# Performance work log

Hardware: AMD Instinct MI355X
Metric: run time of the kernel (lower is better)

Reference implementation:

```python
import jax, jax.numpy as jnp
import numpy as np

B, N, D, H = 2, 2048, 1024, 16
DH = D // H
MASK_VALUE = -1e7


def setup_inputs() -> dict:
    key = jax.random.key(0)
    ks = jax.random.split(key, 8)
    scale = 0.02
    return {
        "queries": jax.random.normal(ks[0], (B, N, D), dtype=jnp.float32),
        "keys": jax.random.normal(ks[1], (B, N, D), dtype=jnp.float32),
        "values": jax.random.normal(ks[2], (B, N, D), dtype=jnp.float32),
        "valid_len": jax.random.randint(ks[3], (B * H,), 1, N + 1, dtype=jnp.int32),
        "Wq": jax.random.normal(ks[4], (D, D), dtype=jnp.float32) * scale,
        "Wk": jax.random.normal(ks[5], (D, D), dtype=jnp.float32) * scale,
        "Wv": jax.random.normal(ks[6], (D, D), dtype=jnp.float32) * scale,
        "Wo": jax.random.normal(ks[7], (D, D), dtype=jnp.float32) * scale,
    }


def reference(queries, keys, values, valid_len, Wq, Wk, Wv, Wo):
    b, n, d = queries.shape
    h, dh = H, d // H

    def split_heads(x):  # (b, n, d) -> (b, h, n, dh)
        return x.reshape(b, n, h, dh).transpose(0, 2, 1, 3)

    q = split_heads(queries @ Wq)
    k = split_heads(keys @ Wk)
    v = split_heads(values @ Wv)

    # (b, h, nq, nk) full score tensor, as in the original naive bmm path
    scores = jnp.einsum("bhqd,bhkd->bhqk", q, k) / jnp.sqrt(jnp.float32(dh))

    # valid_len is 1-D of length b*h; repeat_interleave over queries means the
    # mask depends only on the key index: keep k < valid_len[bh]
    vl = valid_len.reshape(b, h, 1, 1)
    keep = jnp.arange(n)[None, None, None, :] < vl  # (b, h, 1, nk)
    scores = jnp.where(keep, scores, MASK_VALUE)

    attn = jax.nn.softmax(scores, axis=-1)
    heads = jnp.einsum("bhqk,bhkd->bhqd", attn, v)  # (b, h, n, dh)
    out = heads.transpose(0, 2, 1, 3).reshape(b, n, d) @ Wo
    return out
```

## Files before the change

kernel.cpp:

```cpp
#include <hip/hip_runtime.h>

#define B_ 2
#define N_ 2048
#define D_ 1024
#define H_ 16
#define DH_ 64
#define NITEMS 1024

typedef _Float16 half8 __attribute__((ext_vector_type(8)));
typedef _Float16 half4 __attribute__((ext_vector_type(4)));
typedef float f32x4 __attribute__((ext_vector_type(4)));

__device__ __forceinline__ void gl2lds16(const _Float16* g, _Float16* l) {
  __builtin_amdgcn_global_load_lds(
      (const __attribute__((address_space(1))) void*)g,
      (__attribute__((address_space(3))) void*)l, 16, 0, 0);
}

__global__ __launch_bounds__(256) void prep_kernel(
    const float* __restrict__ q, const float* __restrict__ k,
    const float* __restrict__ v, const float* __restrict__ Wq,
    const float* __restrict__ Wk, const float* __restrict__ Wv,
    const float* __restrict__ Wo, const int* __restrict__ vlen,
    _Float16* __restrict__ Xf, _Float16* __restrict__ WtAll,
    int* __restrict__ order) {
  __shared__ float tile[64][65];
  const int bid = blockIdx.x;
  if (bid < 6144) {
    int y = bid >> 11, x = bid & 2047;
    const float* s = (y == 0) ? q : (y == 1) ? k : v;
    _Float16* d = Xf + (size_t)y * ((size_t)B_ * N_ * D_);
    size_t idx = ((size_t)x * 256 + threadIdx.x) * 8;
    float4 a = *(const float4*)(s + idx);
    float4 b = *(const float4*)(s + idx + 4);
    half8 h;
    h[0] = (_Float16)a.x; h[1] = (_Float16)a.y; h[2] = (_Float16)a.z; h[3] = (_Float16)a.w;
    h[4] = (_Float16)b.x; h[5] = (_Float16)b.y; h[6] = (_Float16)b.z; h[7] = (_Float16)b.w;
    *(half8*)(d + idx) = h;
  } else if (bid < 6144 + 1024) {
    int idx = bid - 6144;
    int z = idx >> 8, rem = idx & 255, gy = rem >> 4, gx = rem & 15;
    const float* W = (z == 0) ? Wq : (z == 1) ? Wk : (z == 2) ? Wv : Wo;
    _Float16* Wt = WtAll + (size_t)z * D_ * D_;
    int k0 = gy * 64, n0 = gx * 64;
    int tr = threadIdx.x >> 4, tc = threadIdx.x & 15;
#pragma unroll
    for (int i = 0; i < 4; ++i) {
      int r = tr + i * 16;
      float4 va = *(const float4*)(W + (size_t)(k0 + r) * D_ + n0 + tc * 4);
      tile[r][tc * 4 + 0] = va.x; tile[r][tc * 4 + 1] = va.y;
      tile[r][tc * 4 + 2] = va.z; tile[r][tc * 4 + 3] = va.w;
    }
    __syncthreads();
#pragma unroll
    for (int i = 0; i < 4; ++i) {
      int r = tr + i * 16;
      half4 hv;
      hv[0] = (_Float16)tile[tc * 4 + 0][r];
      hv[1] = (_Float16)tile[tc * 4 + 1][r];
      hv[2] = (_Float16)tile[tc * 4 + 2][r];
      hv[3] = (_Float16)tile[tc * 4 + 3][r];
      *(half4*)(Wt + (size_t)(n0 + r) * D_ + k0 + tc * 4) = hv;
    }
  } else {
    int i = threadIdx.x;
    if (i < B_ * H_) {
      int vi = vlen[i], rank = 0;
      for (int j = 0; j < B_ * H_; ++j) {
        int vj = vlen[j];
        if (vj > vi || (vj == vi && j < i)) ++rank;
      }
      order[rank] = i;
    }
  }
}

#define BK 32

template <int NT, int MODE>
__global__ __launch_bounds__(256) void gemm_f16_kernel(
    const _Float16* __restrict__ Aall, const _Float16* __restrict__ Btall,
    _Float16* __restrict__ ChAll, float* __restrict__ Cf32) {
  constexpr int BN = NT * 32;
  constexpr int K = D_;
  __shared__ __attribute__((aligned(16))) _Float16 As[128 * BK];
  __shared__ __attribute__((aligned(16))) _Float16 Bs[BN * BK];
  const int z = blockIdx.z;
  const _Float16* A  = Aall  + (size_t)z * ((size_t)B_ * N_ * D_);
  const _Float16* Bt = Btall + (size_t)z * ((size_t)D_ * D_);
  _Float16* Chead = ChAll + (size_t)z * ((size_t)B_ * N_ * D_);

  const int tid = threadIdx.x;
  const int m0 = blockIdx.y * 128, n0 = blockIdx.x * BN;
  const int lane = tid & 63, w = tid >> 6;
  const int quad = lane >> 4, l15 = lane & 15;
  const int wm = (w >> 1) * 64, wn = (w & 1) * (BN / 2);
  const int swz = (quad ^ ((l15 >> 1) & 3)) * 8;
  f32x4 acc[4][NT] = {};

  for (int kt = 0; kt < K; kt += BK) {
    if (kt) __syncthreads();
#pragma unroll
    for (int p = 0; p < 2; ++p) {
      int c = p * 256 + tid;
      int row = c >> 2, pg = c & 3;
      int gl = pg ^ ((row >> 1) & 3);
      gl2lds16(A + (size_t)(m0 + row) * K + kt + gl * 8, &As[c * 8]);
    }
#pragma unroll
    for (int p = 0; p < NT / 2; ++p) {
      int c = p * 256 + tid;
      int row = c >> 2, pg = c & 3;
      int gl = pg ^ ((row >> 1) & 3);
      gl2lds16(Bt + (size_t)(n0 + row) * K + kt + gl * 8, &Bs[c * 8]);
    }
    __syncthreads();
    half8 af[4], bf[NT];
#pragma unroll
    for (int mt = 0; mt < 4; ++mt)
      af[mt] = *(const half8*)&As[(wm + mt * 16 + l15) * 32 + swz];
#pragma unroll
    for (int nt = 0; nt < NT; ++nt)
      bf[nt] = *(const half8*)&Bs[(wn + nt * 16 + l15) * 32 + swz];
#pragma unroll
    for (int mt = 0; mt < 4; ++mt)
#pragma unroll
      for (int nt = 0; nt < NT; ++nt)
        acc[mt][nt] = __builtin_amdgcn_mfma_f32_16x16x32_f16(
            af[mt], bf[nt], acc[mt][nt], 0, 0, 0);
  }

#pragma unroll
  for (int mt = 0; mt < 4; ++mt) {
    int mrow = m0 + wm + mt * 16 + quad * 4;
#pragma unroll
    for (int nt = 0; nt < NT; ++nt) {
      int jcol = n0 + wn + nt * 16 + l15;
#pragma unroll
      for (int r = 0; r < 4; ++r) {
        float val = acc[mt][nt][r];
        int m = mrow + r;
        if (MODE == 0) {
          int b = m >> 11, n = m & (N_ - 1);
          int h = jcol >> 6, dh = jcol & (DH_ - 1);
          Chead[((((size_t)(b * H_ + h)) * N_ + n) * DH_) + dh] = (_Float16)val;
        } else {
          Cf32[(size_t)m * D_ + jcol] = val;
        }
      }
    }
  }
}

__global__ __launch_bounds__(256) void transpose_v_kernel(
    const _Float16* __restrict__ Vh, _Float16* __restrict__ VtG) {
  __shared__ float Ls[64][65];
  int bh = blockIdx.y, k0 = blockIdx.x * 64;
  int tid = threadIdx.x;
  const _Float16* src = Vh + (size_t)bh * N_ * DH_;
#pragma unroll
  for (int p = 0; p < 2; ++p) {
    int c = p * 256 + tid, row = c >> 3, pg = c & 7;
    half8 hv = *(const half8*)(src + (size_t)(k0 + row) * DH_ + pg * 8);
#pragma unroll
    for (int u = 0; u < 8; ++u) Ls[row][pg * 8 + u] = (float)hv[u];
  }
  __syncthreads();
  _Float16* dst = VtG + (size_t)bh * N_ * DH_;
#pragma unroll
  for (int p = 0; p < 2; ++p) {
    int c = p * 256 + tid, dh = c >> 3, pg = c & 7;
    half8 hv;
#pragma unroll
    for (int u = 0; u < 8; ++u) hv[u] = (_Float16)Ls[pg * 8 + u][dh];
    *(half8*)(dst + (size_t)dh * N_ + k0 + pg * 8) = hv;
  }
}

__global__ __launch_bounds__(256, 4) void attn_kernel(
    const _Float16* __restrict__ Qh, const _Float16* __restrict__ Kh,
    const _Float16* __restrict__ VtG, const int* __restrict__ vlen,
    _Float16* __restrict__ Hd, const int* __restrict__ order) {
  __shared__ __attribute__((aligned(16))) _Float16 Ks[2][64 * 64];
  __shared__ __attribute__((aligned(16))) _Float16 Vt[2][64 * 64];
  const int tid = threadIdx.x, lane = tid & 63, w = tid >> 6;
  const int quad = lane >> 4, l15 = lane & 15;
  const int sw  = (quad ^ (l15 & 7)) * 8;
  const int sw2 = ((quad + 4) ^ (l15 & 7)) * 8;
  const float sc2 = 0.125f * 1.44269504088896f;
  const half4 ones = {(_Float16)1, (_Float16)1, (_Float16)1, (_Float16)1};

  const int item = blockIdx.x;
  const int bh = order[item >> 5];
  const int q0 = (item & 31) * 64;
  const int b = bh >> 4, h = bh & (H_ - 1);
  const int vl = vlen[bh];
  const int KT = (vl + 63) >> 6;
  const _Float16* Qb = Qh  + (size_t)bh * N_ * DH_;
  const _Float16* Kb = Kh  + (size_t)bh * N_ * DH_;
  const _Float16* Vb = VtG + (size_t)bh * N_ * DH_;

  const half8 qb0 = *(const half8*)(Qb + (size_t)(q0 + w * 16 + l15) * DH_ + quad * 8);
  const half8 qb1 = *(const half8*)(Qb + (size_t)(q0 + w * 16 + l15) * DH_ + 32 + quad * 8);

  half8 kpre[2], vpre[2];
  auto prefetch = [&](int k0k) {
#pragma unroll
    for (int p = 0; p < 2; ++p) {
      int c = p * 256 + tid;
      int row = c >> 3, pg = c & 7;
      kpre[p] = *(const half8*)(Kb + (size_t)(k0k + row) * DH_ + (pg ^ (row & 7)) * 8);
      vpre[p] = *(const half8*)(Vb + (size_t)row * N_ + k0k + pg * 8);
    }
  };
  auto commit = [&](int buf) {
#pragma unroll
    for (int p = 0; p < 2; ++p) {
      int c = p * 256 + tid;
      int row = c >> 3, pg = c & 7;
      *(half8*)&Ks[buf][c * 8] = kpre[p];
      int j0 = (pg * 2) ^ (row & 15), j1 = (pg * 2 + 1) ^ (row & 15);
      half4 lo = {vpre[p][0], vpre[p][1], vpre[p][2], vpre[p][3]};
      half4 hi = {vpre[p][4], vpre[p][5], vpre[p][6], vpre[p][7]};
      *(half4*)&Vt[buf][row * 64 + j0 * 4] = lo;
      *(half4*)&Vt[buf][row * 64 + j1 * 4] = hi;
    }
  };

  prefetch(0);
  commit(0);
  if (KT > 1) prefetch(64);
  __syncthreads();

  f32x4 Oacc[4] = {};
  f32x4 lacc = {};

  for (int kt = 0; kt < KT; ++kt) {
    const int cur = kt & 1;
    if (kt + 1 < KT) commit(1 - cur);
    if (kt + 2 < KT) prefetch((kt + 2) * 64);

    f32x4 s[4];
#pragma unroll
    for (int nt = 0; nt < 4; ++nt) {
      int r = nt * 16 + l15;
      half8 ka0 = *(const half8*)&Ks[cur][r * 64 + sw];
      half8 ka1 = *(const half8*)&Ks[cur][r * 64 + sw2];
      f32x4 c = {};
      c = __builtin_amdgcn_mfma_f32_16x16x32_f16(ka0, qb0, c, 0, 0, 0);
      c = __builtin_amdgcn_mfma_f32_16x16x32_f16(ka1, qb1, c, 0, 0, 0);
      s[nt] = c;
    }
    const int k0k = kt * 64;
    half4 pf[4];
    if (k0k + 64 <= vl) {
#pragma unroll
      for (int nt = 0; nt < 4; ++nt)
#pragma unroll
        for (int r = 0; r < 4; ++r)
          pf[nt][r] = (_Float16)exp2f(s[nt][r] * sc2);
    } else {
#pragma unroll
      for (int nt = 0; nt < 4; ++nt) {
        int keyb = k0k + nt * 16 + quad * 4;
#pragma unroll
        for (int r = 0; r < 4; ++r) {
          float p = exp2f(s[nt][r] * sc2);
          pf[nt][r] = (keyb + r < vl) ? (_Float16)p : (_Float16)0.f;
        }
      }
    }
#pragma unroll
    for (int nt = 0; nt < 4; ++nt) {
      lacc = __builtin_amdgcn_mfma_f32_16x16x16f16(ones, pf[nt], lacc, 0, 0, 0);
#pragma unroll
      for (int dt = 0; dt < 4; ++dt) {
        int dh = dt * 16 + l15;
        half4 va = *(const half4*)&Vt[cur][dh * 64 + (((nt * 4 + quad) ^ l15) << 2)];
        Oacc[dt] = __builtin_amdgcn_mfma_f32_16x16x16f16(va, pf[nt], Oacc[dt], 0, 0, 0);
      }
    }
    __syncthreads();
  }

  float inv_l = 1.0f / lacc[0];
  int q = q0 + w * 16 + l15;
  _Float16* out = Hd + ((size_t)(b * N_ + q)) * D_ + h * DH_;
#pragma unroll
  for (int dt = 0; dt < 4; ++dt) {
    half4 o;
#pragma unroll
    for (int r = 0; r < 4; ++r) o[r] = (_Float16)(Oacc[dt][r] * inv_l);
    *(half4*)(out + dt * 16 + quad * 4) = o;
  }
}

extern "C" void kernel_launch(void* const* d_in, const int* in_sizes, int n_in,
                              void* d_out, int out_size, void* d_ws, size_t ws_size,
                              hipStream_t stream) {
  const float* q  = (const float*)d_in[0];
  const float* k  = (const float*)d_in[1];
  const float* v  = (const float*)d_in[2];
  const int*   vl = (const int*)d_in[3];
  const float* Wq = (const float*)d_in[4];
  const float* Wk = (const float*)d_in[5];
  const float* Wv = (const float*)d_in[6];
  const float* Wo = (const float*)d_in[7];

  const size_t XSZ = (size_t)B_ * N_ * D_;
  const size_t WSZ = (size_t)D_ * D_;
  _Float16* ws = (_Float16*)d_ws;
  _Float16* Xf = ws;
  _Float16* Wt = Xf + 3 * XSZ;
  _Float16* Qh = Wt + 4 * WSZ;
  _Float16* Hd = Qh + 3 * XSZ;
  int* order = (int*)(Hd + XSZ);
  _Float16* VtG = Xf;

  prep_kernel<<<dim3(6144 + 1024 + 1), 256, 0, stream>>>(
      q, k, v, Wq, Wk, Wv, Wo, vl, Xf, Wt, order);

  gemm_f16_kernel<4, 0><<<dim3(D_ / 128, 32, 3), 256, 0, stream>>>(
      Xf, Wt, Qh, nullptr);

  transpose_v_kernel<<<dim3(N_ / 64, B_ * H_), 256, 0, stream>>>(
      Qh + 2 * XSZ, VtG);

  attn_kernel<<<dim3(NITEMS), 256, 0, stream>>>(
      Qh, Qh + XSZ, VtG, vl, Hd, order);

  gemm_f16_kernel<2, 1><<<dim3(D_ / 64, 32, 1), 256, 0, stream>>>(
      Hd, Wt + 3 * WSZ, nullptr, (float*)d_out);
}
```

Measured before the change: 218.6 us.

## Fuse V transpose and softmax scale into QKV GEMM epilogue, permute attention blocks

The QKV projection epilogue now writes V directly in transposed head layout with vectorized half4 stores, which removes the separate transpose kernel launch and its round trip through memory. The softmax scale and log2e factor are folded into Q at store time, so the attention loop drops a multiply per score. Probabilities are packed to f16 with cvt_pkrtz, and attention blocks are visited in a permuted order to balance work across valid lengths. Risks: the diff references z and ChAll, which may not be defined in the unseen GEMM code. Scaling Q before rounding to f16 and using round-toward-zero packing slightly change numerics.

```diff
diff --git a/kernel.cpp b/kernel.cpp
--- a/kernel.cpp
+++ b/kernel.cpp
@@ -9,12 +9,18 @@
 
 typedef _Float16 half8 __attribute__((ext_vector_type(8)));
 typedef _Float16 half4 __attribute__((ext_vector_type(4)));
+typedef _Float16 half2 __attribute__((ext_vector_type(2)));
 typedef float f32x4 __attribute__((ext_vector_type(4)));
 
 __device__ __forceinline__ void gl2lds16(const _Float16* g, _Float16* l) {
   __builtin_amdgcn_global_load_lds(
       (const __attribute__((address_space(1))) void*)g,
       (__attribute__((address_space(3))) void*)l, 16, 0, 0);
+}
+
+__device__ __forceinline__ half2 cvt_pk_f16(float a, float b) {
+  auto r = __builtin_amdgcn_cvt_pkrtz(a, b);
+  return __builtin_bit_cast(half2, r);
 }
 
 __global__ __launch_bounds__(256) void prep_kernel(
@@ -136,44 +142,28 @@
 #pragma unroll
     for (int nt = 0; nt < NT; ++nt) {
       int jcol = n0 + wn + nt * 16 + l15;
-#pragma unroll
-      for (int r = 0; r < 4; ++r) {
-        float val = acc[mt][nt][r];
-        int m = mrow + r;
-        if (MODE == 0) {
-          int b = m >> 11, n = m & (N_ - 1);
-          int h = jcol >> 6, dh = jcol & (DH_ - 1);
-          Chead[((((size_t)(b * H_ + h)) * N_ + n) * DH_) + dh] = (_Float16)val;
+      if (MODE == 0) {
+        int b = mrow >> 11, n = mrow & (N_ - 1);
+        int h = jcol >> 6, dh = jcol & (DH_ - 1);
+        if (z == 2) {
+          half4 o;
+#pragma unroll
+          for (int r = 0; r < 4; ++r) o[r] = (_Float16)acc[mt][nt][r];
+          *(half4*)(ChAll + 2 * (size_t)B_ * N_ * D_ +
+                    ((size_t)(b * H_ + h) * DH_ + dh) * N_ + n) = o;
         } else {
-          Cf32[(size_t)m * D_ + jcol] = val;
+          const float scl = (z == 0) ? 0.18033688011112042f : 1.0f;
+#pragma unroll
+          for (int r = 0; r < 4; ++r)
+            Chead[((((size_t)(b * H_ + h)) * N_ + n + r) * DH_) + dh] =
+                (_Float16)(acc[mt][nt][r] * scl);
         }
-      }
-    }
-  }
-}
-
-__global__ __launch_bounds__(256) void transpose_v_kernel(
-    const _Float16* __restrict__ Vh, _Float16* __restrict__ VtG) {
-  __shared__ float Ls[64][65];
-  int bh = blockIdx.y, k0 = blockIdx.x * 64;
-  int tid = threadIdx.x;
-  const _Float16* src = Vh + (size_t)bh * N_ * DH_;
-#pragma unroll
-  for (int p = 0; p < 2; ++p) {
-    int c = p * 256 + tid, row = c >> 3, pg = c & 7;
-    half8 hv = *(const half8*)(src + (size_t)(k0 + row) * DH_ + pg * 8);
-#pragma unroll
-    for (int u = 0; u < 8; ++u) Ls[row][pg * 8 + u] = (float)hv[u];
-  }
-  __syncthreads();
-  _Float16* dst = VtG + (size_t)bh * N_ * DH_;
-#pragma unroll
-  for (int p = 0; p < 2; ++p) {
-    int c = p * 256 + tid, dh = c >> 3, pg = c & 7;
-    half8 hv;
-#pragma unroll
-    for (int u = 0; u < 8; ++u) hv[u] = (_Float16)Ls[pg * 8 + u][dh];
-    *(half8*)(dst + (size_t)dh * N_ + k0 + pg * 8) = hv;
+      } else {
+#pragma unroll
+        for (int r = 0; r < 4; ++r)
+          Cf32[(size_t)(mrow + r) * D_ + jcol] = acc[mt][nt][r];
+      }
+    }
   }
 }
 
@@ -187,10 +177,9 @@
   const int quad = lane >> 4, l15 = lane & 15;
   const int sw  = (quad ^ (l15 & 7)) * 8;
   const int sw2 = ((quad + 4) ^ (l15 & 7)) * 8;
-  const float sc2 = 0.125f * 1.44269504088896f;
   const half4 ones = {(_Float16)1, (_Float16)1, (_Float16)1, (_Float16)1};
 
-  const int item = blockIdx.x;
+  const int item = (blockIdx.x * 331) & (NITEMS - 1);
   const int bh = order[item >> 5];
   const int q0 = (item & 31) * 64;
   const int b = bh >> 4, h = bh & (H_ - 1);
@@ -255,17 +244,18 @@
     half4 pf[4];
     if (k0k + 64 <= vl) {
 #pragma unroll
-      for (int nt = 0; nt < 4; ++nt)
-#pragma unroll
-        for (int r = 0; r < 4; ++r)
-          pf[nt][r] = (_Float16)exp2f(s[nt][r] * sc2);
+      for (int nt = 0; nt < 4; ++nt) {
+        half2 lo = cvt_pk_f16(exp2f(s[nt][0]), exp2f(s[nt][1]));
+        half2 hi = cvt_pk_f16(exp2f(s[nt][2]), exp2f(s[nt][3]));
+        pf[nt] = __builtin_shufflevector(lo, hi, 0, 1, 2, 3);
+      }
     } else {
 #pragma unroll
       for (int nt = 0; nt < 4; ++nt) {
         int keyb = k0k + nt * 16 + quad * 4;
 #pragma unroll
         for (int r = 0; r < 4; ++r) {
-          float p = exp2f(s[nt][r] * sc2);
+          float p = exp2f(s[nt][r]);
           pf[nt][r] = (keyb + r < vl) ? (_Float16)p : (_Float16)0.f;
         }
       }
@@ -315,7 +305,6 @@
   _Float16* Qh = Wt + 4 * WSZ;
   _Float16* Hd = Qh + 3 * XSZ;
   int* order = (int*)(Hd + XSZ);
-  _Float16* VtG = Xf;
 
   prep_kernel<<<dim3(6144 + 1024 + 1), 256, 0, stream>>>(
       q, k, v, Wq, Wk, Wv, Wo, vl, Xf, Wt, order);
@@ -323,11 +312,8 @@
   gemm_f16_kernel<4, 0><<<dim3(D_ / 128, 32, 3), 256, 0, stream>>>(
       Xf, Wt, Qh, nullptr);
 
-  transpose_v_kernel<<<dim3(N_ / 64, B_ * H_), 256, 0, stream>>>(
-      Qh + 2 * XSZ, VtG);
-
   attn_kernel<<<dim3(NITEMS), 256, 0, stream>>>(
-      Qh, Qh + XSZ, VtG, vl, Hd, order);
+      Qh, Qh + XSZ, Qh + 2 * XSZ, vl, Hd, order);
 
   gemm_f16_kernel<2, 1><<<dim3(D_ / 64, 32, 1), 256, 0, stream>>>(
       Hd, Wt + 3 * WSZ, nullptr, (float*)d_out);
```

After: 224.6 us. 1.03x slower.
